# Kernel tuning notes

Hardware: AMD Instinct MI355X
Metric: run time of the kernel (lower is better)

The kernel has to match this reference:

```python
import jax, jax.numpy as jnp
import numpy as np

CHUNK, OVERLAP = 4096, 1024
STRIDE = CHUNK - OVERLAP            # 3072
NFFT, HOP = 1024, 256
F = NFFT // 2 + 1                   # 513
NF = (CHUNK - NFFT) // HOP + 1      # 13 frames per chunk (center=False)
H, E = 256, 128
B, C, T = 8, 1, 480000


def setup_inputs() -> dict:
    key = jax.random.key(0)
    ks = jax.random.split(key, 8)
    s = lambda d: 1.0 / np.sqrt(d)
    return {
        "audio": jax.random.normal(ks[0], (B, C, T), jnp.float32),
        "emb_table": jax.random.normal(ks[1], (16, E), jnp.float32) * 0.1,
        "gru_wx": jax.random.normal(ks[2], (F + E, 3 * H), jnp.float32) * s(F + E),
        "gru_wh": jax.random.normal(ks[3], (H, 3 * H), jnp.float32) * s(H),
        "gru_b": jnp.zeros((3 * H,), jnp.float32),
        "proj_w": jax.random.normal(ks[4], (H, 2 * F), jnp.float32) * s(H),
        "proj_b": jnp.zeros((2 * F,), jnp.float32),
        "effect_id": jax.random.randint(ks[5], (B,), 0, 16),
    }


def _hann(n):
    return (0.5 - 0.5 * jnp.cos(2.0 * jnp.pi * jnp.arange(n) / n)).astype(jnp.float32)


def _film(mag, emb, gru_wx, gru_wh, gru_b, proj_w, proj_b):
    # mag: [B, C, K, NF, F]; emb: [B, E]
    b, c, k, nf, f = mag.shape
    emb_b = jnp.broadcast_to(emb[:, None, None, None, :], (b, c, k, nf, E))
    x = jnp.concatenate([mag, emb_b], axis=-1).reshape(b * c * k, nf, f + E)
    xg = x @ gru_wx                                   # [M, NF, 3H]
    h0 = jnp.zeros((b * c * k, H), mag.dtype)

    def step(h, xg_t):
        hg = h @ gru_wh + gru_b
        z = jax.nn.sigmoid(xg_t[:, :H] + hg[:, :H])
        r = jax.nn.sigmoid(xg_t[:, H:2 * H] + hg[:, H:2 * H])
        n = jnp.tanh(xg_t[:, 2 * H:] + r * hg[:, 2 * H:])
        h = (1.0 - z) * n + z * h
        return h, h

    _, hs = jax.lax.scan(step, h0, jnp.swapaxes(xg, 0, 1))  # [NF, M, H]
    hs = jnp.swapaxes(hs, 0, 1)                              # [M, NF, H]
    gb = hs @ proj_w + proj_b                                # [M, NF, 2F]
    gamma, beta = gb[..., :F], gb[..., F:]
    gamma = gamma.reshape(b, c, k, nf, f)
    beta = beta.reshape(b, c, k, nf, f)
    return gamma * mag + beta


def reference(audio, emb_table, gru_wx, gru_wh, gru_b, proj_w, proj_b, effect_id):
    win = _hann(NFFT)
    emb = emb_table[effect_id]                              # [B, E]

    t = audio.shape[-1]
    n_chunks = -(-t // STRIDE)                              # 157
    t_pad = (n_chunks - 1) * STRIDE + CHUNK
    xp = jnp.pad(audio, ((0, 0), (0, 0), (0, t_pad - t)))

    cidx = jnp.arange(n_chunks)[:, None] * STRIDE + jnp.arange(CHUNK)  # [K, CHUNK]
    chunks = xp[..., cidx]                                  # [B, C, K, CHUNK]

    fidx = jnp.arange(NF)[:, None] * HOP + jnp.arange(NFFT)  # [NF, NFFT]
    frames = chunks[..., fidx] * win                         # [B, C, K, NF, NFFT]
    spec = jnp.fft.rfft(frames, axis=-1)                     # [B, C, K, NF, F]

    mag = jnp.abs(spec)
    phase = jnp.angle(spec)
    mod_mag = _film(mag, emb, gru_wx, gru_wh, gru_b, proj_w, proj_b)
    comp = jax.lax.complex(mod_mag * jnp.cos(phase), mod_mag * jnp.sin(phase))

    y = jnp.fft.irfft(comp, n=NFFT, axis=-1) * win           # [B, C, K, NF, NFFT]
    rec = jnp.zeros_like(chunks).at[..., fidx].add(y)        # OLA within chunk
    wsum = jnp.zeros((CHUNK,), jnp.float32).at[fidx].add(win ** 2)
    rec = rec / jnp.maximum(wsum, 1e-8)

    out = jnp.zeros_like(xp).at[..., cidx].add(rec)          # OLA across chunks
    return out[..., :t]
```

## Files before the change

kernel.cpp:

```cpp
#include <hip/hip_runtime.h>
#include <math.h>

#define T_LEN    480000
#define NB       8
#define NK       157
#define CHUNKSZ  4096
#define STRIDESZ 3072
#define NFFT_SZ  1024
#define HOP_SZ   256
#define NFREQ    513
#define NFR      13
#define HDIM     256
#define EDIM     128
#define GDIM     768
#define PDIM     1026
#define FR_STRIDE 1026
#define NFRAMES  (NB*NK*NFR)
#define NCHUNKS  (NB*NK)
#define KCF      2041

#define XG_KS    17
#define XG_NB    3
#define PJ_KS    8
#define PJ_NB    5
#define GRU_CT   5

#define TWO_PI_D 6.283185307179586

typedef short bf16x8 __attribute__((ext_vector_type(8)));
typedef float f32x4  __attribute__((ext_vector_type(4)));

__device__ __forceinline__ void split_bf16(float v, short& hi, short& lo) {
  unsigned u = __float_as_uint(v);
  hi = (short)(u >> 16);
  float fh = __uint_as_float(u & 0xFFFF0000u);
  float res = v - fh;
  lo = (short)(__float_as_uint(res) >> 16);
}

__device__ __forceinline__ unsigned short f2bf(float v) {
  unsigned u = __float_as_uint(v);
  u += 0x7FFFu + ((u >> 16) & 1u);
  return (unsigned short)(u >> 16);
}
__device__ __forceinline__ float bf2f(unsigned short b) {
  return __uint_as_float(((unsigned)b) << 16);
}

__device__ __forceinline__ void fft1024(float* re, float* im,
                                        const float* twc, const float* tws,
                                        int tid, float dir) {
  #pragma unroll
  for (int s = 1; s <= 9; s += 2) {
    int half = 1 << (s - 1);
    int p   = tid & (half - 1);
    int grp = tid >> (s - 1);
    int i0  = grp * 4 * half + p;
    int i1  = i0 + half;
    int i2  = i0 + 2 * half;
    int i3  = i0 + 3 * half;
    float r0 = re[i0], q0 = im[i0], r1 = re[i1], q1 = im[i1];
    float r2 = re[i2], q2 = im[i2], r3 = re[i3], q3 = im[i3];
    int qa = p << (10 - s);
    float ca = twc[qa], sa = dir * tws[qa];
    float tr = ca * r1 - sa * q1, ti = ca * q1 + sa * r1;
    float u0r = r0 + tr, u0i = q0 + ti;
    float u1r = r0 - tr, u1i = q0 - ti;
    tr = ca * r3 - sa * q3; ti = ca * q3 + sa * r3;
    float u2r = r2 + tr, u2i = q2 + ti;
    float u3r = r2 - tr, u3i = q2 - ti;
    int qb = p << (9 - s);
    int qc = (p + half) << (9 - s);
    float cb = twc[qb], sb = dir * tws[qb];
    float cc = twc[qc], sc = dir * tws[qc];
    tr = cb * u2r - sb * u2i; ti = cb * u2i + sb * u2r;
    re[i0] = u0r + tr; im[i0] = u0i + ti;
    re[i2] = u0r - tr; im[i2] = u0i - ti;
    tr = cc * u3r - sc * u3i; ti = cc * u3i + sc * u3r;
    re[i1] = u1r + tr; im[i1] = u1i + ti;
    re[i3] = u1r - tr; im[i3] = u1i - ti;
    __syncthreads();
  }
}

__global__ void k_tables(float* __restrict__ win, float* __restrict__ wsinv,
                         float* __restrict__ twc, float* __restrict__ tws) {
  int tid = threadIdx.x;
  for (int i = tid; i < NFFT_SZ; i += 256) {
    double w = 0.5 - 0.5 * cos((TWO_PI_D / (double)NFFT_SZ) * (double)i);
    win[i] = (float)w;
  }
  for (int i = tid; i < 512; i += 256) {
    double th = (TWO_PI_D / (double)NFFT_SZ) * (double)i;
    twc[i] = (float)cos(th);
    tws[i] = (float)sin(th);
  }
  for (int pc = tid; pc < CHUNKSZ; pc += 256) {
    int t1 = min(NFR - 1, pc >> 8);
    int t0 = (pc > NFFT_SZ - 1) ? ((pc - 768) >> 8) : 0;
    float ws = 0.f;
    for (int tt = t0; tt <= t1; ++tt) {
      int n = pc - tt * HOP_SZ;
      double w = 0.5 - 0.5 * cos((TWO_PI_D / (double)NFFT_SZ) * (double)n);
      float wf = (float)w;
      ws += wf * wf;
    }
    wsinv[pc] = 1.0f / fmaxf(ws, 1e-8f);
  }
}

__global__ void k_prep(const float* __restrict__ wx,
                       short* __restrict__ wxb_hi, short* __restrict__ wxb_lo) {
  int id = blockIdx.x * 256 + threadIdx.x;
  if (id >= XG_NB * XG_KS * 256) return;
  int nb  = id / (XG_KS * 256);
  int ks  = (id / 256) % XG_KS;
  int col = id % 256;
  int col_g = nb * 256 + col;
  size_t base = (size_t)id * 32;
  for (int j = 0; j < 32; ++j) {
    int k_g = ks * 32 + j;
    float v = wx[(size_t)k_g * GDIM + col_g];
    short hi, lo;
    split_bf16(v, hi, lo);
    wxb_hi[base + j] = hi;
    wxb_lo[base + j] = lo;
  }
}

__global__ void k_prep_wht(const float* __restrict__ wh, float4* __restrict__ whT4) {
  int id = blockIdx.x * 256 + threadIdx.x;
  if (id >= 64 * GDIM) return;
  int k4  = id / GDIM;
  int col = id % GDIM;
  whT4[id] = make_float4(wh[(size_t)(k4 * 4 + 0) * GDIM + col],
                         wh[(size_t)(k4 * 4 + 1) * GDIM + col],
                         wh[(size_t)(k4 * 4 + 2) * GDIM + col],
                         wh[(size_t)(k4 * 4 + 3) * GDIM + col]);
}

__global__ void k_prep_pw(const float* __restrict__ pw,
                          short* __restrict__ pwb_hi, short* __restrict__ pwb_lo) {
  int id = blockIdx.x * 256 + threadIdx.x;
  if (id >= PJ_NB * PJ_KS * 256) return;
  int nb  = id / (PJ_KS * 256);
  int ks  = (id / 256) % PJ_KS;
  int col = id % 256;
  int col_g = nb * 256 + col;
  size_t base = (size_t)id * 32;
  for (int j = 0; j < 32; ++j) {
    int k_g = ks * 32 + j;
    float v = (col_g < PDIM) ? pw[(size_t)k_g * PDIM + col_g] : 0.f;
    short hi, lo;
    split_bf16(v, hi, lo);
    pwb_hi[base + j] = hi;
    pwb_lo[base + j] = lo;
  }
}

__global__ void k_embxg(const float* __restrict__ emb_table, const int* __restrict__ effect_id,
                        const float* __restrict__ wx, float* __restrict__ embxg) {
  int b = blockIdx.x;
  int tid = threadIdx.x;
  int e_id = effect_id[b];
  const float* ev = emb_table + (size_t)e_id * EDIM;
  #pragma unroll
  for (int j = 0; j < 3; ++j) {
    int col = tid + 256 * j;
    float acc = 0.f;
    #pragma unroll 4
    for (int e = 0; e < EDIM; ++e)
      acc += ev[e] * wx[(size_t)(NFREQ + e) * GDIM + col];
    embxg[(size_t)b * GDIM + col] = acc;
  }
}

__global__ void k_stft(const float* __restrict__ audio, const float* __restrict__ win,
                       const float* __restrict__ gtwc, const float* __restrict__ gtws,
                       unsigned* __restrict__ spec) {
  int fr = blockIdx.x;
  int b   = fr / (NK * NFR);
  int rem = fr % (NK * NFR);
  int k = rem / NFR, t = rem % NFR;
  int tid = threadIdx.x;
  __shared__ float xin[NFFT_SZ];
  __shared__ float re[NFFT_SZ], im[NFFT_SZ];
  __shared__ float twc[512], tws[512];
  for (int i = tid; i < 512; i += 256) { twc[i] = gtwc[i]; tws[i] = gtws[i]; }
  int start = k * STRIDESZ + t * HOP_SZ;
  for (int i = tid; i < NFFT_SZ; i += 256) {
    int pos = start + i;
    float v = (pos < T_LEN) ? audio[b * T_LEN + pos] : 0.f;
    xin[i] = v * win[i];
  }
  __syncthreads();
  for (int i = tid; i < NFFT_SZ; i += 256) {
    int rv = (int)(__brev((unsigned)i) >> 22);
    re[i] = xin[rv];
    im[i] = 0.f;
  }
  __syncthreads();
  fft1024(re, im, twc, tws, tid, -1.f);
  unsigned* sp = spec + (size_t)fr * (FR_STRIDE / 2);
  for (int f = tid; f < NFREQ; f += 256) {
    unsigned pr = f2bf(re[f]);
    unsigned pi = f2bf(im[f]);
    sp[f] = (pi << 16) | pr;
  }
}

__global__ __launch_bounds__(256) void k_xg(
    const unsigned* __restrict__ spec, const float* __restrict__ embxg,
    const short* __restrict__ wxb_hi, const short* __restrict__ wxb_lo,
    float* __restrict__ xg) {
  int nb  = blockIdx.x % XG_NB;
  int mb  = blockIdx.x / XG_NB;
  int fr0 = mb * 64;
  int tid = threadIdx.x;
  int lane = tid & 63;
  int wv   = tid >> 6;

  __shared__ __align__(16) short lsA[2][64 * 40];
  __shared__ __align__(16) short lsB[2][256 * 40];

  f32x4 acc[4][4];
  #pragma unroll
  for (int i = 0; i < 4; ++i)
    #pragma unroll
    for (int j = 0; j < 4; ++j)
      acc[i][j] = (f32x4){0.f, 0.f, 0.f, 0.f};

  int lrow = lane & 15;
  int lk8  = (lane >> 4) * 8;

  for (int ks = 0; ks < XG_KS; ++ks) {
    int k0 = ks * 32;
    {
      int f = tid >> 2, q = tid & 3;
      int fr = fr0 + f;
      short hi[8], lo[8];
      #pragma unroll
      for (int j = 0; j < 8; ++j) {
        int bg = k0 + q * 8 + j;
        float m = 0.f;
        if (fr < NFRAMES && bg <= 512) {
          unsigned pv = spec[(size_t)fr * (FR_STRIDE / 2) + bg];
          float rr = bf2f((unsigned short)(pv & 0xFFFFu));
          float ii = bf2f((unsigned short)(pv >> 16));
          m = sqrtf(rr * rr + ii * ii);
        }
        split_bf16(m, hi[j], lo[j]);
      }
      int off = f * 40 + q * 8;
      *(bf16x8*)&lsA[0][off] = *(bf16x8*)hi;
      *(bf16x8*)&lsA[1][off] = *(bf16x8*)lo;
    }
    {
      const short* gh = wxb_hi + (((size_t)nb * XG_KS + ks) * 256 + tid) * 32;
      const short* gl = wxb_lo + (((size_t)nb * XG_KS + ks) * 256 + tid) * 32;
      int off = tid * 40;
      #pragma unroll
      for (int i = 0; i < 4; ++i) {
        *(bf16x8*)&lsB[0][off + 8 * i] = *(const bf16x8*)(gh + 8 * i);
        *(bf16x8*)&lsB[1][off + 8 * i] = *(const bf16x8*)(gl + 8 * i);
      }
    }
    __syncthreads();
    bf16x8 aH[4], aL[4], bH[4], bL[4];
    #pragma unroll
    for (int mt = 0; mt < 4; ++mt) {
      int off = (16 * mt + lrow) * 40 + lk8;
      aH[mt] = *(const bf16x8*)&lsA[0][off];
      aL[mt] = *(const bf16x8*)&lsA[1][off];
    }
    #pragma unroll
    for (int nt = 0; nt < 4; ++nt) {
      int col = wv * 64 + nt * 16 + lrow;
      int off = col * 40 + lk8;
      bH[nt] = *(const bf16x8*)&lsB[0][off];
      bL[nt] = *(const bf16x8*)&lsB[1][off];
    }
    #pragma unroll
    for (int mt = 0; mt < 4; ++mt)
      #pragma unroll
      for (int nt = 0; nt < 4; ++nt) {
        acc[mt][nt] = __builtin_amdgcn_mfma_f32_16x16x32_bf16(aH[mt], bH[nt], acc[mt][nt], 0, 0, 0);
        acc[mt][nt] = __builtin_amdgcn_mfma_f32_16x16x32_bf16(aH[mt], bL[nt], acc[mt][nt], 0, 0, 0);
        acc[mt][nt] = __builtin_amdgcn_mfma_f32_16x16x32_bf16(aL[mt], bH[nt], acc[mt][nt], 0, 0, 0);
      }
    __syncthreads();
  }

  int ncol0 = nb * 256 + wv * 64;
  #pragma unroll
  for (int mt = 0; mt < 4; ++mt) {
    #pragma unroll
    for (int r = 0; r < 4; ++r) {
      int fr = fr0 + mt * 16 + (lane >> 4) * 4 + r;
      if (fr < NFRAMES) {
        int b = fr / KCF;
        #pragma unroll
        for (int nt = 0; nt < 4; ++nt) {
          int col = ncol0 + nt * 16 + (lane & 15);
          xg[(size_t)fr * GDIM + col] = acc[mt][nt][r] + embxg[(size_t)b * GDIM + col];
        }
      }
    }
  }
}

__global__ __launch_bounds__(768) void k_gru(
    const float* __restrict__ xg, const float4* __restrict__ whT4,
    const float* __restrict__ bias, float* __restrict__ hs) {
  int c0 = blockIdx.x * GRU_CT;
  int tid = threadIdx.x;
  __shared__ __align__(16) float h[GRU_CT][HDIM];
  __shared__ float hg[GRU_CT][GDIM];
  float* hflat = &h[0][0];
  for (int i = tid; i < GRU_CT * HDIM; i += 768) hflat[i] = 0.f;
  float bcol = bias[tid];
  __syncthreads();
  for (int t = 0; t < NFR; ++t) {
    float acc[GRU_CT];
    #pragma unroll
    for (int c = 0; c < GRU_CT; ++c) acc[c] = bcol;
    const float4* wp = whT4 + tid;
    #pragma unroll 2
    for (int k = 0; k < HDIM; k += 4) {
      float4 w = *wp;
      wp += GDIM;
      #pragma unroll
      for (int c = 0; c < GRU_CT; ++c) {
        float4 hv = *(const float4*)&h[c][k];
        acc[c] += hv.x * w.x + hv.y * w.y + hv.z * w.z + hv.w * w.w;
      }
    }
    #pragma unroll
    for (int c = 0; c < GRU_CT; ++c) hg[c][tid] = acc[c];
    __syncthreads();
    for (int i = tid; i < GRU_CT * HDIM; i += 768) {
      int c = i >> 8, u = i & 255;
      int cb = c0 + c;
      if (cb < NCHUNKS) {
        const float* xgt = xg + (size_t)(cb * NFR + t) * GDIM;
        float z = 1.f / (1.f + expf(-(xgt[u] + hg[c][u])));
        float r = 1.f / (1.f + expf(-(xgt[u + 256] + hg[c][u + 256])));
        float n = tanhf(xgt[u + 512] + r * hg[c][u + 512]);
        float hn = (1.f - z) * n + z * h[c][u];
        h[c][u] = hn;
        hs[(size_t)(cb * NFR + t) * HDIM + u] = hn;
      }
    }
    __syncthreads();
  }
}

__global__ __launch_bounds__(256) void k_proj(
    const float* __restrict__ hs, const short* __restrict__ pwb_hi,
    const short* __restrict__ pwb_lo, const float* __restrict__ pb,
    unsigned short* __restrict__ gb) {
  int nb  = blockIdx.x % PJ_NB;
  int mb  = blockIdx.x / PJ_NB;
  int fr0 = mb * 64;
  int tid = threadIdx.x;
  int lane = tid & 63;
  int wv   = tid >> 6;

  __shared__ __align__(16) short lsA[2][64 * 40];
  __shared__ __align__(16) short lsB[2][256 * 40];

  f32x4 acc[4][4];
  #pragma unroll
  for (int i = 0; i < 4; ++i)
    #pragma unroll
    for (int j = 0; j < 4; ++j)
      acc[i][j] = (f32x4){0.f, 0.f, 0.f, 0.f};

  int lrow = lane & 15;
  int lk8  = (lane >> 4) * 8;

  for (int ks = 0; ks < PJ_KS; ++ks) {
    {
      int f = tid >> 2, q = tid & 3;
      int fr = fr0 + f;
      float v[8];
      if (fr < NFRAMES) {
        const float* src = hs + (size_t)fr * HDIM + ks * 32 + q * 8;
        float4 v0 = *(const float4*)src;
        float4 v1 = *(const float4*)(src + 4);
        v[0]=v0.x; v[1]=v0.y; v[2]=v0.z; v[3]=v0.w;
        v[4]=v1.x; v[5]=v1.y; v[6]=v1.z; v[7]=v1.w;
      } else {
        #pragma unroll
        for (int j = 0; j < 8; ++j) v[j] = 0.f;
      }
      short hi[8], lo[8];
      #pragma unroll
      for (int j = 0; j < 8; ++j) split_bf16(v[j], hi[j], lo[j]);
      int off = f * 40 + q * 8;
      *(bf16x8*)&lsA[0][off] = *(bf16x8*)hi;
      *(bf16x8*)&lsA[1][off] = *(bf16x8*)lo;
    }
    {
      const short* gh = pwb_hi + (((size_t)nb * PJ_KS + ks) * 256 + tid) * 32;
      const short* gl = pwb_lo + (((size_t)nb * PJ_KS + ks) * 256 + tid) * 32;
      int off = tid * 40;
      #pragma unroll
      for (int i = 0; i < 4; ++i) {
        *(bf16x8*)&lsB[0][off + 8 * i] = *(const bf16x8*)(gh + 8 * i);
        *(bf16x8*)&lsB[1][off + 8 * i] = *(const bf16x8*)(gl + 8 * i);
      }
    }
    __syncthreads();
    bf16x8 aH[4], aL[4], bH[4], bL[4];
    #pragma unroll
    for (int mt = 0; mt < 4; ++mt) {
      int off = (16 * mt + lrow) * 40 + lk8;
      aH[mt] = *(const bf16x8*)&lsA[0][off];
      aL[mt] = *(const bf16x8*)&lsA[1][off];
    }
    #pragma unroll
    for (int nt = 0; nt < 4; ++nt) {
      int col = wv * 64 + nt * 16 + lrow;
      int off = col * 40 + lk8;
      bH[nt] = *(const bf16x8*)&lsB[0][off];
      bL[nt] = *(const bf16x8*)&lsB[1][off];
    }
    #pragma unroll
    for (int mt = 0; mt < 4; ++mt)
      #pragma unroll
      for (int nt = 0; nt < 4; ++nt) {
        acc[mt][nt] = __builtin_amdgcn_mfma_f32_16x16x32_bf16(aH[mt], bH[nt], acc[mt][nt], 0, 0, 0);
        acc[mt][nt] = __builtin_amdgcn_mfma_f32_16x16x32_bf16(aH[mt], bL[nt], acc[mt][nt], 0, 0, 0);
        acc[mt][nt] = __builtin_amdgcn_mfma_f32_16x16x32_bf16(aL[mt], bH[nt], acc[mt][nt], 0, 0, 0);
      }
    __syncthreads();
  }

  int ncol0 = nb * 256 + wv * 64;
  float pbv[4];
  int cols[4];
  #pragma unroll
  for (int nt = 0; nt < 4; ++nt) {
    cols[nt] = ncol0 + nt * 16 + (lane & 15);
    pbv[nt] = (cols[nt] < PDIM) ? pb[cols[nt]] : 0.f;
  }
  #pragma unroll
  for (int mt = 0; mt < 4; ++mt) {
    #pragma unroll
    for (int r = 0; r < 4; ++r) {
      int fr = fr0 + mt * 16 + (lane >> 4) * 4 + r;
      if (fr < NFRAMES) {
        #pragma unroll
        for (int nt = 0; nt < 4; ++nt) {
          if (cols[nt] < PDIM)
            gb[(size_t)fr * PDIM + cols[nt]] = f2bf(acc[mt][nt][r] + pbv[nt]);
        }
      }
    }
  }
}

__global__ void k_istft(unsigned* __restrict__ spec, const unsigned short* __restrict__ gb,
                        const float* __restrict__ win, const float* __restrict__ wsinv,
                        const float* __restrict__ gtwc, const float* __restrict__ gtws) {
  int fr = blockIdx.x;
  int tid = threadIdx.x;
  int t = fr % NFR;
  __shared__ float sre[NFREQ], sim[NFREQ];
  __shared__ float re[NFFT_SZ], im[NFFT_SZ];
  __shared__ float twc[512], tws[512];
  for (int i = tid; i < 512; i += 256) { twc[i] = gtwc[i]; tws[i] = gtws[i]; }
  unsigned* sp = spec + (size_t)fr * (FR_STRIDE / 2);
  const unsigned short* gbrow = gb + (size_t)fr * PDIM;
  for (int f = tid; f < NFREQ; f += 256) {
    unsigned pv = sp[f];
    float r  = bf2f((unsigned short)(pv & 0xFFFFu));
    float iv = bf2f((unsigned short)(pv >> 16));
    float mag = sqrtf(r * r + iv * iv);
    float gamma = bf2f(gbrow[f]);
    float beta  = bf2f(gbrow[NFREQ + f]);
    float mm = gamma * mag + beta;
    float nr, ni;
    if (mag > 0.f) {
      float s = mm / mag;
      nr = r * s; ni = iv * s;
    } else {
      nr = mm; ni = 0.f;
    }
    sre[f] = nr;
    sim[f] = (f == 0 || f == NFREQ - 1) ? 0.f : ni;
  }
  __syncthreads();
  for (int i = tid; i < NFFT_SZ; i += 256) {
    int src = (int)(__brev((unsigned)i) >> 22);
    float r, iv;
    if (src <= 512) { r = sre[src]; iv = sim[src]; }
    else            { r = sre[NFFT_SZ - src]; iv = -sim[NFFT_SZ - src]; }
    re[i] = r; im[i] = iv;
  }
  __syncthreads();
  fft1024(re, im, twc, tws, tid, +1.f);
  for (int i2 = tid; i2 < 512; i2 += 256) {
    int ia = 2 * i2, ib = 2 * i2 + 1;
    float ya = re[ia] * (1.0f / (float)NFFT_SZ) * win[ia] * wsinv[t * HOP_SZ + ia];
    float yb = re[ib] * (1.0f / (float)NFFT_SZ) * win[ib] * wsinv[t * HOP_SZ + ib];
    unsigned pa = f2bf(ya);
    unsigned pbp = f2bf(yb);
    sp[i2] = (pbp << 16) | pa;
  }
}

__global__ void k_gather(const unsigned short* __restrict__ ybuf, float* __restrict__ out) {
  int gid = blockIdx.x * 256 + threadIdx.x;
  if (gid >= NB * T_LEN) return;
  int b = gid / T_LEN, pos = gid % T_LEN;
  float acc = 0.f;
  int k_hi = min(NK - 1, pos / STRIDESZ);
  int k_lo = (pos >= CHUNKSZ) ? ((pos - (CHUNKSZ - 1) + (STRIDESZ - 1)) / STRIDESZ) : 0;
  for (int k = k_lo; k <= k_hi; ++k) {
    int pc = pos - k * STRIDESZ;
    int t1 = min(NFR - 1, pc >> 8);
    int t0 = (pc > NFFT_SZ - 1) ? ((pc - 768) >> 8) : 0;
    int frbase = (b * NK + k) * NFR;
    for (int tt = t0; tt <= t1; ++tt) {
      acc += bf2f(ybuf[(size_t)(frbase + tt) * FR_STRIDE + (pc - tt * HOP_SZ)]);
    }
  }
  out[gid] = acc;
}

extern "C" void kernel_launch(void* const* d_in, const int* in_sizes, int n_in,
                              void* d_out, int out_size, void* d_ws, size_t ws_size,
                              hipStream_t stream) {
  const float* audio     = (const float*)d_in[0];
  const float* emb_table = (const float*)d_in[1];
  const float* gru_wx    = (const float*)d_in[2];
  const float* gru_wh    = (const float*)d_in[3];
  const float* gru_b     = (const float*)d_in[4];
  const float* proj_w    = (const float*)d_in[5];
  const float* proj_b    = (const float*)d_in[6];
  const int*   effect_id = (const int*)d_in[7];
  float* out = (float*)d_out;

  char* base = (char*)d_ws;
  size_t off = 0;
  auto alloc = [&](size_t bytes) { char* p = base + off; off = (off + bytes + 255) & ~(size_t)255; return p; };
  unsigned* spec   = (unsigned*)alloc((size_t)NFRAMES * FR_STRIDE * 2);
  float*    xg     = (float*)   alloc((size_t)NFRAMES * GDIM * 4);
  float*    hs     = (float*)   alloc((size_t)NFRAMES * HDIM * 4);
  float*    win    = (float*)   alloc(NFFT_SZ * 4);
  float*    wsinv  = (float*)   alloc(CHUNKSZ * 4);
  float*    twc    = (float*)   alloc(512 * 4);
  float*    tws    = (float*)   alloc(512 * 4);
  float*    embxg  = (float*)   alloc(NB * GDIM * 4);
  short*    wxb_hi = (short*)   alloc((size_t)XG_NB * XG_KS * 256 * 32 * 2);
  short*    wxb_lo = (short*)   alloc((size_t)XG_NB * XG_KS * 256 * 32 * 2);
  short*    pwb_hi = (short*)   alloc((size_t)PJ_NB * PJ_KS * 256 * 32 * 2);
  short*    pwb_lo = (short*)   alloc((size_t)PJ_NB * PJ_KS * 256 * 32 * 2);
  float4*   whT4   = (float4*)  alloc((size_t)64 * GDIM * 16);
  unsigned short* gb = (unsigned short*)xg;

  k_tables  <<<1, 256, 0, stream>>>(win, wsinv, twc, tws);
  k_embxg   <<<NB, 256, 0, stream>>>(emb_table, effect_id, gru_wx, embxg);
  k_prep    <<<(XG_NB * XG_KS * 256 + 255) / 256, 256, 0, stream>>>(gru_wx, wxb_hi, wxb_lo);
  k_prep_wht<<<(64 * GDIM + 255) / 256, 256, 0, stream>>>(gru_wh, whT4);
  k_prep_pw <<<(PJ_NB * PJ_KS * 256 + 255) / 256, 256, 0, stream>>>(proj_w, pwb_hi, pwb_lo);
  k_stft    <<<NFRAMES, 256, 0, stream>>>(audio, win, twc, tws, spec);
  k_xg      <<<256 * XG_NB, 256, 0, stream>>>(spec, embxg, wxb_hi, wxb_lo, xg);
  k_gru     <<<(NCHUNKS + GRU_CT - 1) / GRU_CT, 768, 0, stream>>>(xg, whT4, gru_b, hs);
  k_proj    <<<256 * PJ_NB, 256, 0, stream>>>(hs, pwb_hi, pwb_lo, proj_b, gb);
  k_istft   <<<NFRAMES, 256, 0, stream>>>(spec, gb, win, wsinv, twc, tws);
  k_gather  <<<(NB * T_LEN + 255) / 256, 256, 0, stream>>>((const unsigned short*)spec, out);
}
```

Measured before the change: 620.0 us.

## Use packed real FFT via half-length complex FFT, two frames per block

The STFT and ISTFT kernels now compute each 1024-point real transform as a 512-point complex FFT on even/odd-packed samples, with a post/pre twiddle split step. Each 256-thread block processes two frames, so the grid is halved. This roughly halves butterfly work and shared-memory traffic per frame and drops one radix stage and barrier. In exchange it adds the split/merge passes and a separate radix-2 final stage. NFRAMES being even is relied on.

```diff
diff --git a/kernel.cpp b/kernel.cpp
--- a/kernel.cpp
+++ b/kernel.cpp
@@ -47,20 +47,22 @@
   return __uint_as_float(((unsigned)b) << 16);
 }
 
-__device__ __forceinline__ void fft1024(float* re, float* im,
-                                        const float* twc, const float* tws,
-                                        int tid, float dir) {
+__device__ __forceinline__ void fft512x2(float (*re)[512], float (*im)[512],
+                                         const float* twc, const float* tws,
+                                         int tid, float dir) {
+  int q = tid >> 7;
+  int j = tid & 127;
   #pragma unroll
-  for (int s = 1; s <= 9; s += 2) {
+  for (int s = 1; s <= 7; s += 2) {
     int half = 1 << (s - 1);
-    int p   = tid & (half - 1);
-    int grp = tid >> (s - 1);
+    int p   = j & (half - 1);
+    int grp = j >> (s - 1);
     int i0  = grp * 4 * half + p;
     int i1  = i0 + half;
     int i2  = i0 + 2 * half;
     int i3  = i0 + 3 * half;
-    float r0 = re[i0], q0 = im[i0], r1 = re[i1], q1 = im[i1];
-    float r2 = re[i2], q2 = im[i2], r3 = re[i3], q3 = im[i3];
+    float r0 = re[q][i0], q0 = im[q][i0], r1 = re[q][i1], q1 = im[q][i1];
+    float r2 = re[q][i2], q2 = im[q][i2], r3 = re[q][i3], q3 = im[q][i3];
     int qa = p << (10 - s);
     float ca = twc[qa], sa = dir * tws[qa];
     float tr = ca * r1 - sa * q1, ti = ca * q1 + sa * r1;
@@ -74,11 +76,27 @@
     float cb = twc[qb], sb = dir * tws[qb];
     float cc = twc[qc], sc = dir * tws[qc];
     tr = cb * u2r - sb * u2i; ti = cb * u2i + sb * u2r;
-    re[i0] = u0r + tr; im[i0] = u0i + ti;
-    re[i2] = u0r - tr; im[i2] = u0i - ti;
+    re[q][i0] = u0r + tr; im[q][i0] = u0i + ti;
+    re[q][i2] = u0r - tr; im[q][i2] = u0i - ti;
     tr = cc * u3r - sc * u3i; ti = cc * u3i + sc * u3r;
-    re[i1] = u1r + tr; im[i1] = u1i + ti;
-    re[i3] = u1r - tr; im[i3] = u1i - ti;
+    re[q][i1] = u1r + tr; im[q][i1] = u1i + ti;
+    re[q][i3] = u1r - tr; im[q][i3] = u1i - ti;
+    __syncthreads();
+  }
+  {
+    int p = tid;
+    int qd = p << 1;
+    float c = twc[qd], sn = dir * tws[qd];
+    #pragma unroll
+    for (int f = 0; f < 2; ++f) {
+      int i1 = p, i2 = p + 256;
+      float r2 = re[f][i2], q2 = im[f][i2];
+      float tr = c * r2 - sn * q2;
+      float ti = c * q2 + sn * r2;
+      float r1 = re[f][i1], q1 = im[f][i1];
+      re[f][i2] = r1 - tr; im[f][i2] = q1 - ti;
+      re[f][i1] = r1 + tr; im[f][i1] = q1 + ti;
+    }
     __syncthreads();
   }
 }
@@ -178,34 +196,50 @@
 __global__ void k_stft(const float* __restrict__ audio, const float* __restrict__ win,
                        const float* __restrict__ gtwc, const float* __restrict__ gtws,
                        unsigned* __restrict__ spec) {
-  int fr = blockIdx.x;
-  int b   = fr / (NK * NFR);
-  int rem = fr % (NK * NFR);
-  int k = rem / NFR, t = rem % NFR;
+  int fr0 = blockIdx.x * 2;
   int tid = threadIdx.x;
-  __shared__ float xin[NFFT_SZ];
-  __shared__ float re[NFFT_SZ], im[NFFT_SZ];
+  __shared__ float xin[2][NFFT_SZ];
+  __shared__ float re[2][512], im[2][512];
   __shared__ float twc[512], tws[512];
   for (int i = tid; i < 512; i += 256) { twc[i] = gtwc[i]; tws[i] = gtws[i]; }
-  int start = k * STRIDESZ + t * HOP_SZ;
-  for (int i = tid; i < NFFT_SZ; i += 256) {
-    int pos = start + i;
+  for (int i = tid; i < 2 * NFFT_SZ; i += 256) {
+    int q = i >> 10, ii = i & 1023;
+    int fr = fr0 + q;
+    int b   = fr / KCF;
+    int rem = fr % KCF;
+    int k = rem / NFR, t = rem % NFR;
+    int pos = k * STRIDESZ + t * HOP_SZ + ii;
     float v = (pos < T_LEN) ? audio[b * T_LEN + pos] : 0.f;
-    xin[i] = v * win[i];
+    xin[q][ii] = v * win[ii];
   }
   __syncthreads();
-  for (int i = tid; i < NFFT_SZ; i += 256) {
-    int rv = (int)(__brev((unsigned)i) >> 22);
-    re[i] = xin[rv];
-    im[i] = 0.f;
+  for (int i = tid; i < 1024; i += 256) {
+    int q = i >> 9, n = i & 511;
+    int rv = (int)(__brev((unsigned)n) >> 23);
+    re[q][n] = xin[q][2 * rv];
+    im[q][n] = xin[q][2 * rv + 1];
   }
   __syncthreads();
-  fft1024(re, im, twc, tws, tid, -1.f);
-  unsigned* sp = spec + (size_t)fr * (FR_STRIDE / 2);
-  for (int f = tid; f < NFREQ; f += 256) {
-    unsigned pr = f2bf(re[f]);
-    unsigned pi = f2bf(im[f]);
-    sp[f] = (pi << 16) | pr;
+  fft512x2(re, im, twc, tws, tid, -1.f);
+  for (int i = tid; i < 1024; i += 256) {
+    int q = i >> 9, k = i & 511;
+    int m = (512 - k) & 511;
+    float zr = re[q][k],  zi = im[q][k];
+    float mr = re[q][m],  mi = -im[q][m];
+    float xer = 0.5f * (zr + mr), xei = 0.5f * (zi + mi);
+    float dr  = 0.5f * (zr - mr), di  = 0.5f * (zi - mi);
+    float xor_ = di, xoi = -dr;
+    float c = twc[k], s = tws[k];
+    float Xr = xer + c * xor_ + s * xoi;
+    float Xi = xei + c * xoi - s * xor_;
+    unsigned* sp = spec + (size_t)(fr0 + q) * (FR_STRIDE / 2);
+    sp[k] = (((unsigned)f2bf(Xi)) << 16) | (unsigned)f2bf(Xr);
+  }
+  if (tid < 2) {
+    int q = tid;
+    float Xr = re[q][0] - im[q][0];
+    unsigned* sp = spec + (size_t)(fr0 + q) * (FR_STRIDE / 2);
+    sp[512] = (((unsigned)f2bf(0.f)) << 16) | (unsigned)f2bf(Xr);
   }
 }
 
@@ -464,20 +498,21 @@
 __global__ void k_istft(unsigned* __restrict__ spec, const unsigned short* __restrict__ gb,
                         const float* __restrict__ win, const float* __restrict__ wsinv,
                         const float* __restrict__ gtwc, const float* __restrict__ gtws) {
-  int fr = blockIdx.x;
+  int fr0 = blockIdx.x * 2;
   int tid = threadIdx.x;
-  int t = fr % NFR;
-  __shared__ float sre[NFREQ], sim[NFREQ];
-  __shared__ float re[NFFT_SZ], im[NFFT_SZ];
+  __shared__ float sre[2][NFREQ], sim[2][NFREQ];
+  __shared__ float re[2][512], im[2][512];
   __shared__ float twc[512], tws[512];
   for (int i = tid; i < 512; i += 256) { twc[i] = gtwc[i]; tws[i] = gtws[i]; }
-  unsigned* sp = spec + (size_t)fr * (FR_STRIDE / 2);
-  const unsigned short* gbrow = gb + (size_t)fr * PDIM;
-  for (int f = tid; f < NFREQ; f += 256) {
-    unsigned pv = sp[f];
+  for (int i = tid; i < 2 * NFREQ; i += 256) {
+    int q = (i >= NFREQ) ? 1 : 0;
+    int f = i - q * NFREQ;
+    int fr = fr0 + q;
+    unsigned pv = spec[(size_t)fr * (FR_STRIDE / 2) + f];
     float r  = bf2f((unsigned short)(pv & 0xFFFFu));
     float iv = bf2f((unsigned short)(pv >> 16));
     float mag = sqrtf(r * r + iv * iv);
+    const unsigned short* gbrow = gb + (size_t)fr * PDIM;
     float gamma = bf2f(gbrow[f]);
     float beta  = bf2f(gbrow[NFREQ + f]);
     float mm = gamma * mag + beta;
@@ -488,26 +523,34 @@
     } else {
       nr = mm; ni = 0.f;
     }
-    sre[f] = nr;
-    sim[f] = (f == 0 || f == NFREQ - 1) ? 0.f : ni;
+    sre[q][f] = nr;
+    sim[q][f] = (f == 0 || f == NFREQ - 1) ? 0.f : ni;
   }
   __syncthreads();
-  for (int i = tid; i < NFFT_SZ; i += 256) {
-    int src = (int)(__brev((unsigned)i) >> 22);
-    float r, iv;
-    if (src <= 512) { r = sre[src]; iv = sim[src]; }
-    else            { r = sre[NFFT_SZ - src]; iv = -sim[NFFT_SZ - src]; }
-    re[i] = r; im[i] = iv;
+  for (int i = tid; i < 1024; i += 256) {
+    int q = i >> 9, n = i & 511;
+    int k = (int)(__brev((unsigned)n) >> 23);
+    float Xr = sre[q][k],       Xi = sim[q][k];
+    float Mr = sre[q][512 - k], Mi = -sim[q][512 - k];
+    float xer = 0.5f * (Xr + Mr), xei = 0.5f * (Xi + Mi);
+    float dr  = 0.5f * (Xr - Mr), di  = 0.5f * (Xi - Mi);
+    float c = twc[k], s = tws[k];
+    float xor_ = c * dr - s * di;
+    float xoi  = c * di + s * dr;
+    re[q][n] = xer - xoi;
+    im[q][n] = xei + xor_;
   }
   __syncthreads();
-  fft1024(re, im, twc, tws, tid, +1.f);
-  for (int i2 = tid; i2 < 512; i2 += 256) {
-    int ia = 2 * i2, ib = 2 * i2 + 1;
-    float ya = re[ia] * (1.0f / (float)NFFT_SZ) * win[ia] * wsinv[t * HOP_SZ + ia];
-    float yb = re[ib] * (1.0f / (float)NFFT_SZ) * win[ib] * wsinv[t * HOP_SZ + ib];
-    unsigned pa = f2bf(ya);
-    unsigned pbp = f2bf(yb);
-    sp[i2] = (pbp << 16) | pa;
+  fft512x2(re, im, twc, tws, tid, +1.f);
+  for (int i = tid; i < 1024; i += 256) {
+    int q = i >> 9, n = i & 511;
+    int fr = fr0 + q;
+    int t = fr % NFR;
+    int ia = 2 * n, ib = 2 * n + 1;
+    float ya = re[q][n] * (1.0f / 512.0f) * win[ia] * wsinv[t * HOP_SZ + ia];
+    float yb = im[q][n] * (1.0f / 512.0f) * win[ib] * wsinv[t * HOP_SZ + ib];
+    unsigned* sp = spec + (size_t)fr * (FR_STRIDE / 2);
+    sp[n] = (((unsigned)f2bf(yb)) << 16) | (unsigned)f2bf(ya);
   }
 }
 
@@ -566,10 +609,10 @@
   k_prep    <<<(XG_NB * XG_KS * 256 + 255) / 256, 256, 0, stream>>>(gru_wx, wxb_hi, wxb_lo);
   k_prep_wht<<<(64 * GDIM + 255) / 256, 256, 0, stream>>>(gru_wh, whT4);
   k_prep_pw <<<(PJ_NB * PJ_KS * 256 + 255) / 256, 256, 0, stream>>>(proj_w, pwb_hi, pwb_lo);
-  k_stft    <<<NFRAMES, 256, 0, stream>>>(audio, win, twc, tws, spec);
+  k_stft    <<<NFRAMES / 2, 256, 0, stream>>>(audio, win, twc, tws, spec);
   k_xg      <<<256 * XG_NB, 256, 0, stream>>>(spec, embxg, wxb_hi, wxb_lo, xg);
   k_gru     <<<(NCHUNKS + GRU_CT - 1) / GRU_CT, 768, 0, stream>>>(xg, whT4, gru_b, hs);
   k_proj    <<<256 * PJ_NB, 256, 0, stream>>>(hs, pwb_hi, pwb_lo, proj_b, gb);
-  k_istft   <<<NFRAMES, 256, 0, stream>>>(spec, gb, win, wsinv, twc, tws);
+  k_istft   <<<NFRAMES / 2, 256, 0, stream>>>(spec, gb, win, wsinv, twc, tws);
   k_gather  <<<(NB * T_LEN + 255) / 256, 256, 0, stream>>>((const unsigned short*)spec, out);
 }
```

Result: faster. 541.5 us (-12.7%).
